# Optimization experiments

Hardware: AMD Instinct MI355X
Metric: run time of the kernel (lower is better)

## Reference

```python
import jax, jax.numpy as jnp
import numpy as np

K = 8  # search_range in sample_wise_recolor
BIG = 1e30


def setup_inputs() -> dict:
    key = jax.random.key(0)
    ks = jax.random.split(key, 6)
    L, N = 16384, 10000  # L: upsampled candidate voxels (multiple of 8), N: target points
    pred_F = jax.random.normal(ks[0], (L,), jnp.float32)
    cand_xyz = jax.random.normal(ks[1], (L, 3), jnp.float32) * 50.0
    cand_rgb = jax.random.uniform(ks[2], (L, 3), jnp.float32)
    tgt_xyz = jax.random.normal(ks[3], (N, 3), jnp.float32) * 50.0
    tgt_rgb = jax.random.uniform(ks[4], (N, 3), jnp.float32)
    keep_target = jax.random.randint(ks[5], (L,), 0, 2, jnp.int32)
    return {"pred_F": pred_F, "cand_xyz": cand_xyz, "cand_rgb": cand_rgb,
            "tgt_xyz": tgt_xyz, "tgt_rgb": tgt_rgb, "keep_target": keep_target,
            "points_num": 8192}


def _get_keep(pred, points_num):
    # local-max mask over groups of 8 children (scatter of per-row argmax)
    L = pred.shape[0]
    p8 = pred.reshape(-1, 8)
    rows = jnp.arange(p8.shape[0])
    is_local_max = jnp.zeros(p8.shape, dtype=bool).at[rows, jnp.argmax(p8, axis=1)].set(True).reshape(-1)
    # kthvalue over the non-local-max subset: local-max entries pushed to +inf so the
    # k-th smallest of the full sorted array equals the k-th smallest of the subset.
    k = L - points_num  # static python int
    vals = jnp.where(is_local_max, jnp.inf, pred)
    threshold = jnp.sort(vals)[k - 1]
    return (pred > threshold) | is_local_max


def _pairwise_sqdist(a, b):
    # a: [P,3], b: [Q,3] -> [P,Q] squared distances
    a2 = jnp.sum(a * a, axis=1)
    b2 = jnp.sum(b * b, axis=1)
    d2 = a2[:, None] + b2[None, :] - 2.0 * (a @ b.T)
    return jnp.maximum(d2, 0.0)


def _recolor_loss(cand_xyz, rgb, keep, tgt_xyz, tgt_rgb):
    L = cand_xyz.shape[0]
    N = tgt_xyz.shape[0]
    d2 = _pairwise_sqdist(tgt_xyz, cand_xyz)  # [N, L]

    # ---- recolor_backward: KNN from each target point into kept candidates ----
    d_masked = jnp.where(keep[None, :], d2, BIG)
    neg_d, idx = jax.lax.top_k(-d_masked, K)  # [N, K]
    d = -neg_d
    zero_mask = d == 0.0
    min_mask = (d == jnp.min(d, axis=1, keepdims=True)) & ~jnp.any(zero_mask, axis=1)[:, None]
    w = jnp.where(min_mask, 1.0 / jnp.sqrt(jnp.maximum(d, 1e-30)), 0.0)  # [N, K]

    flat_idx = idx.reshape(-1)
    num = jnp.zeros((L, 3), rgb.dtype).at[flat_idx].add((tgt_rgb[:, None, :] * w[:, :, None]).reshape(-1, 3))
    den = jnp.zeros((L,), rgb.dtype).at[flat_idx].add(w.reshape(-1))
    has_den = den != 0.0
    recolored = jnp.where(has_den[:, None], num / jnp.where(has_den, den, 1.0)[:, None], 0.0)

    # exact-match (zero-distance) targets overwrite; scatter with safe out-of-range dummy row
    safe_idx = jnp.where(zero_mask, idx, L).reshape(-1)
    tgt_exp = jnp.broadcast_to(tgt_rgb[:, None, :], (N, K, 3)).reshape(-1, 3)
    recolored = jnp.concatenate([recolored, jnp.zeros((1, 3), rgb.dtype)], 0).at[safe_idx].set(tgt_exp)[:L]
    empty = jnp.concatenate([~has_den, jnp.zeros((1,), bool)], 0).at[safe_idx].set(False)[:L]
    empty = empty & keep  # only kept candidates matter

    # ---- recolor_forward: kept candidates with no color yet pull from nearest targets ----
    neg_df, idxf = jax.lax.top_k(-d2.T, K)  # [L, K]
    df = -neg_df
    mf = df == jnp.min(df, axis=1, keepdims=True)
    rec_fwd = jnp.sum(tgt_rgb[idxf] * mf[:, :, None], axis=1) / jnp.sum(mf, axis=1, keepdims=True).astype(rgb.dtype)
    recolored = jnp.where(empty[:, None], rec_fwd, recolored)

    # L1 loss over kept candidates only; recolor target is no-grad in the original
    recolored = jax.lax.stop_gradient(recolored)
    return jnp.sum(jnp.where(keep[:, None], jnp.abs(rgb - recolored), 0.0))


def reference(pred_F, cand_xyz, cand_rgb, tgt_xyz, tgt_rgb, keep_target, points_num):
    keep = _get_keep(jax.lax.stop_gradient(pred_F), points_num)  # @torch.no_grad
    # coord recon loss: BCE-with-logits, reduction='sum'
    t = keep_target.astype(pred_F.dtype)
    coord_loss = jnp.sum(jnp.maximum(pred_F, 0.0) - pred_F * t + jnp.log1p(jnp.exp(-jnp.abs(pred_F))))
    # inverse_transform_for_color in training mode: x * 255
    rgb = cand_rgb * 255.0
    rgb_loss = _recolor_loss(cand_xyz, rgb, keep, tgt_xyz, tgt_rgb)
    return jnp.stack([coord_loss, rgb_loss])
```

## Files before the change

### kernel.cpp

```cpp
#include <hip/hip_runtime.h>
#include <hip/hip_bf16.h>


#define SCAN_T 256
typedef unsigned long long ull;

__global__ __launch_bounds__(256) void k_prep(
    const float* __restrict__ pred, const float* __restrict__ txyz,
    float4* __restrict__ ttile, float4* __restrict__ numden,
    int* __restrict__ zerohit, ull* __restrict__ tmin, ull* __restrict__ fmin,
    unsigned int* __restrict__ key, unsigned char* __restrict__ islm,
    int* __restrict__ counters, float* __restrict__ out, int L, int N) {
  int gidx = blockIdx.x * 256 + threadIdx.x;
  int gsz = (int)gridDim.x * 256;
  for (int i = gidx; i < N; i += gsz) {
    float x = txyz[3*i], y = txyz[3*i+1], z = txyz[3*i+2];
    ttile[i] = make_float4(x, y, z, fmaf(x, x, fmaf(y, y, z * z)));
    tmin[i] = ~0ull;
  }
  for (int i = gidx; i < L; i += gsz) {
    numden[i] = make_float4(0.f, 0.f, 0.f, 0.f);
    zerohit[i] = 0;
    fmin[i] = ~0ull;
  }
  if (gidx < 8) counters[gidx] = 0;
  if (gidx < 2) out[gidx] = 0.f;
  int ngroups = L >> 3;
  for (int g = gidx; g < ngroups; g += gsz) {
    const float4* pv = (const float4*)pred + (size_t)g * 2;
    float4 a = pv[0], b = pv[1];
    float v[8] = {a.x, a.y, a.z, a.w, b.x, b.y, b.z, b.w};
    int bi = 0; float bv = v[0];
    #pragma unroll
    for (int j = 1; j < 8; ++j) if (v[j] > bv) { bv = v[j]; bi = j; }
    unsigned int kk[8];
    ull lmpack = 0ull;
    #pragma unroll
    for (int j = 0; j < 8; ++j) {
      unsigned int fb = __float_as_uint(v[j]);
      unsigned int mk = (fb & 0x80000000u) ? ~fb : (fb | 0x80000000u);
      if (j == bi) { mk = 0xFF800000u; lmpack |= 1ull << (8 * j); }
      kk[j] = mk;
    }
    ((uint4*)key)[g*2]   = make_uint4(kk[0], kk[1], kk[2], kk[3]);
    ((uint4*)key)[g*2+1] = make_uint4(kk[4], kk[5], kk[6], kk[7]);
    *(ull*)(islm + (size_t)g * 8) = lmpack;
  }
}

__device__ __forceinline__ void select_bin(
    unsigned int* hist, int nb, unsigned int rank,
    unsigned int* sB, unsigned int* sR, int tid) {
  if (tid < 64) {
    int g = nb >> 6;
    unsigned int sum = 0;
    for (int j = 0; j < g; ++j) sum += hist[tid * g + j];
    unsigned int incl = sum;
    for (int o = 1; o < 64; o <<= 1) {
      unsigned int v = __shfl_up(incl, o);
      if (tid >= o) incl += v;
    }
    unsigned int excl = incl - sum;
    bool cond = (rank >= excl) && (rank < incl);
    unsigned long long bal = __ballot(cond);
    int first = __ffsll((long long)bal) - 1;
    if (tid == first) {
      unsigned int r = rank - excl, cum = 0;
      for (int j = 0; j < g; ++j) {
        unsigned int c = hist[tid * g + j];
        if (r < cum + c) { *sB = (unsigned int)(tid * g + j); *sR = r - cum; break; }
        cum += c;
      }
    }
  }
}

__global__ __launch_bounds__(256) void k_sel(
    const unsigned int* __restrict__ key, const int* __restrict__ pnum_p,
    float* __restrict__ thr_out, int L) {
  __shared__ unsigned int hist[2048];
  __shared__ unsigned int sB, sR;
  int tid = threadIdx.x;
  unsigned int rank = (unsigned int)(L - pnum_p[0] - 1);
  const uint4* k4 = (const uint4*)key;
  int n4 = L >> 2;
  for (int b = tid; b < 2048; b += 256) hist[b] = 0u;
  __syncthreads();
  for (int i = tid; i < n4; i += 256) {
    uint4 v = k4[i];
    atomicAdd(&hist[v.x >> 21], 1u); atomicAdd(&hist[v.y >> 21], 1u);
    atomicAdd(&hist[v.z >> 21], 1u); atomicAdd(&hist[v.w >> 21], 1u);
  }
  __syncthreads();
  select_bin(hist, 2048, rank, &sB, &sR, tid);
  __syncthreads();
  unsigned int B1 = sB, R1 = sR;
  for (int b = tid; b < 2048; b += 256) hist[b] = 0u;
  __syncthreads();
  for (int i = tid; i < n4; i += 256) {
    uint4 v = k4[i];
    if ((v.x >> 21) == B1) atomicAdd(&hist[(v.x >> 10) & 2047u], 1u);
    if ((v.y >> 21) == B1) atomicAdd(&hist[(v.y >> 10) & 2047u], 1u);
    if ((v.z >> 21) == B1) atomicAdd(&hist[(v.z >> 10) & 2047u], 1u);
    if ((v.w >> 21) == B1) atomicAdd(&hist[(v.w >> 10) & 2047u], 1u);
  }
  __syncthreads();
  select_bin(hist, 2048, R1, &sB, &sR, tid);
  __syncthreads();
  unsigned int B2 = sB, R2 = sR;
  for (int b = tid; b < 1024; b += 256) hist[b] = 0u;
  __syncthreads();
  unsigned int top22 = (B1 << 11) | B2;
  for (int i = tid; i < n4; i += 256) {
    uint4 v = k4[i];
    if ((v.x >> 10) == top22) atomicAdd(&hist[v.x & 1023u], 1u);
    if ((v.y >> 10) == top22) atomicAdd(&hist[v.y & 1023u], 1u);
    if ((v.z >> 10) == top22) atomicAdd(&hist[v.z & 1023u], 1u);
    if ((v.w >> 10) == top22) atomicAdd(&hist[v.w & 1023u], 1u);
  }
  __syncthreads();
  select_bin(hist, 1024, R2, &sB, &sR, tid);
  __syncthreads();
  if (tid == 0) {
    unsigned int fkey = (B1 << 21) | (B2 << 10) | sB;
    unsigned int fb = (fkey & 0x80000000u) ? (fkey & 0x7FFFFFFFu) : ~fkey;
    thr_out[0] = __uint_as_float(fb);
  }
}

__global__ __launch_bounds__(256) void k_keepc(
    const float* __restrict__ pred, const unsigned char* __restrict__ islm,
    const float* __restrict__ thr_p, const float* __restrict__ cxyz,
    const int* __restrict__ ktgt, int* __restrict__ keep,
    float4* __restrict__ klist, int* __restrict__ kidx,
    int* __restrict__ counters, float* __restrict__ out, int L) {
  int i = blockIdx.x * 256 + threadIdx.x;
  float thr = thr_p[0];
  float term = 0.f;
  if (i < L) {
    float p = pred[i];
    bool kp = (p > thr) || islm[i];
    keep[i] = kp ? 1 : 0;
    if (kp) {
      int pos = atomicAdd(&counters[0], 1);
      float x = cxyz[3*i], y = cxyz[3*i+1], z = cxyz[3*i+2];
      klist[pos] = make_float4(x, y, z, fmaf(x, x, fmaf(y, y, z * z)));
      kidx[pos] = i;
    }
    float t = (float)ktgt[i];
    term = fmaxf(p, 0.f) - p * t + log1pf(expf(-fabsf(p)));
  }
  for (int o = 32; o > 0; o >>= 1) term += __shfl_down(term, o);
  if ((threadIdx.x & 63) == 0) atomicAdd(&out[0], term);
}

__global__ __launch_bounds__(SCAN_T) void k_scan2(
    const float* __restrict__ txyz, const float4* __restrict__ klist,
    const int* __restrict__ kidx, const float4* __restrict__ ttile,
    const int* __restrict__ counters, ull* __restrict__ tmin,
    ull* __restrict__ fmin, int L, int N, int YB) {
  __shared__ float4 tile[SCAN_T];
  int tid = threadIdx.x, x = blockIdx.x, y = blockIdx.y;
  int kc = counters[0];

  if (y < YB) {
    int c0 = y * 512;
    if (x * 256 >= N || c0 >= kc) return;
    int c1 = min(c0 + 512, kc);
    int t = x * 256 + tid;
    bool act = t < N;
    float tx = 0.f, ty = 0.f, tz = 0.f;
    if (act) { tx = txyz[3*t]; ty = txyz[3*t+1]; tz = txyz[3*t+2]; }
    float ntx = -2.f * tx, nty = -2.f * ty, ntz = -2.f * tz;
    float best = 3e38f; int bpos = -1;
    for (int tb = c0; tb < c1; tb += SCAN_T) {
      int cnt = min(SCAN_T, c1 - tb);
      if (tid < cnt) tile[tid] = klist[tb + tid];
      __syncthreads();
      #pragma unroll 8
      for (int c = 0; c < cnt; ++c) {
        float4 cd = tile[c];
        float d = fmaf(ntx, cd.x, cd.w);
        d = fmaf(nty, cd.y, d);
        d = fmaf(ntz, cd.z, d);
        if (d < best) { best = d; bpos = tb + c; }
      }
      __syncthreads();
    }
    if (act && bpos >= 0) {
      float4 cd = klist[bpos];
      float dx = tx - cd.x, dy = ty - cd.y, dz = tz - cd.z;
      float dtrue = fmaf(dx, dx, fmaf(dy, dy, dz * dz));
      ull pack = ((ull)__float_as_uint(dtrue) << 32) | (unsigned int)kidx[bpos];
      atomicMin(&tmin[t], pack);
    }
  } else {
    int t0 = (y - YB) * 512;
    if (x * 256 >= kc) return;
    int t1 = min(t0 + 512, N);
    int e = x * 256 + tid;
    bool act = e < kc;
    float cx = 0.f, cy = 0.f, cz = 0.f, c2 = 0.f;
    int l = 0;
    if (act) {
      float4 cd = klist[e];
      cx = cd.x; cy = cd.y; cz = cd.z; c2 = cd.w;
      l = kidx[e];
    }
    float ncx = -2.f * cx, ncy = -2.f * cy, ncz = -2.f * cz;
    float best = 3e38f; int bidx = 0;
    for (int tb = t0; tb < t1; tb += SCAN_T) {
      int cnt = min(SCAN_T, t1 - tb);
      if (tid < cnt) tile[tid] = ttile[tb + tid];
      __syncthreads();
      #pragma unroll 8
      for (int c = 0; c < cnt; ++c) {
        float4 td = tile[c];
        float d = fmaf(ncx, td.x, td.w);
        d = fmaf(ncy, td.y, d);
        d = fmaf(ncz, td.z, d);
        if (d < best) { best = d; bidx = tb + c; }
      }
      __syncthreads();
    }
    if (act) {
      float dkey = fmaxf(best + c2, 0.f);
      ull pack = ((ull)__float_as_uint(dkey) << 32) | (unsigned int)bidx;
      atomicMin(&fmin[l], pack);
    }
  }
}

__global__ __launch_bounds__(256) void k_scatter(
    const float* __restrict__ trgb, const ull* __restrict__ tmin,
    float4* __restrict__ numden, int* __restrict__ zerohit,
    float4* __restrict__ zcolor, int N) {
  int t = blockIdx.x * 256 + threadIdx.x;
  if (t >= N) return;
  ull pack = tmin[t];
  float d = __uint_as_float((unsigned int)(pack >> 32));
  int idx = (int)(pack & 0xFFFFFFFFull);
  float r = trgb[3*t], g = trgb[3*t+1], b = trgb[3*t+2];
  if (d == 0.0f) {
    zerohit[idx] = 1;
    zcolor[idx] = make_float4(r, g, b, 0.f);
  } else {
    float w = 1.0f / sqrtf(fmaxf(d, 1e-30f));
    atomicAdd(&numden[idx].x, r * w);
    atomicAdd(&numden[idx].y, g * w);
    atomicAdd(&numden[idx].z, b * w);
    atomicAdd(&numden[idx].w, w);
  }
}

__global__ __launch_bounds__(256) void k_loss(
    const float* __restrict__ crgb, const float* __restrict__ trgb,
    const int* __restrict__ keep, const float4* __restrict__ numden,
    const int* __restrict__ zerohit, const float4* __restrict__ zcolor,
    const ull* __restrict__ fmin, float* __restrict__ out, int L) {
  int l = blockIdx.x * 256 + threadIdx.x;
  float loss = 0.f;
  if (l < L && keep[l]) {
    float rr, rg, rb;
    if (zerohit[l]) {
      float4 z = zcolor[l]; rr = z.x; rg = z.y; rb = z.z;
    } else {
      float4 nd = numden[l];
      if (nd.w != 0.f) { rr = nd.x / nd.w; rg = nd.y / nd.w; rb = nd.z / nd.w; }
      else {
        int ti = (int)(fmin[l] & 0xFFFFFFFFull);
        rr = trgb[3*ti]; rg = trgb[3*ti+1]; rb = trgb[3*ti+2];
      }
    }
    float sr = crgb[3*l]*255.f, sg = crgb[3*l+1]*255.f, sb = crgb[3*l+2]*255.f;
    loss = fabsf(sr - rr) + fabsf(sg - rg) + fabsf(sb - rb);
  }
  for (int o = 32; o > 0; o >>= 1) loss += __shfl_down(loss, o);
  if ((threadIdx.x & 63) == 0) atomicAdd(&out[1], loss);
}

extern "C" void kernel_launch(void* const* d_in, const int* in_sizes, int n_in,
                              void* d_out, int out_size, void* d_ws, size_t ws_size,
                              hipStream_t stream) {
  const float* pred = (const float*)d_in[0];
  const float* cxyz = (const float*)d_in[1];
  const float* crgb = (const float*)d_in[2];
  const float* txyz = (const float*)d_in[3];
  const float* trgb = (const float*)d_in[4];
  const int*   ktgt = (const int*)d_in[5];
  const int*   pnum = (const int*)d_in[6];
  int L = in_sizes[0];
  int N = in_sizes[3] / 3;

  char* ws = (char*)d_ws;
  size_t off = 0;
  float4* klist  = (float4*)(ws + off);   off += (size_t)L * 16;
  float4* ttile  = (float4*)(ws + off);   off += (size_t)((N + 3) & ~3) * 16;
  float4* numden = (float4*)(ws + off);   off += (size_t)L * 16;
  float4* zcolor = (float4*)(ws + off);   off += (size_t)L * 16;
  unsigned int* key = (unsigned int*)(ws + off); off += (size_t)L * 4;
  ull* tmin      = (ull*)(ws + off);      off += (size_t)((N + 1) & ~1) * 8;
  ull* fmin      = (ull*)(ws + off);      off += (size_t)L * 8;
  int* keep      = (int*)(ws + off);      off += (size_t)L * 4;
  int* kidx      = (int*)(ws + off);      off += (size_t)L * 4;
  int* zerohit   = (int*)(ws + off);      off += (size_t)L * 4;
  float* thr_slot = (float*)(ws + off);   off += 16;
  int* counters  = (int*)(ws + off);      off += 256;
  unsigned char* islm = (unsigned char*)(ws + off); off += ((size_t)L + 15) & ~15ull;
  float* out = (float*)d_out;

  int nbL = (L + 255) / 256;
  int nbN = (N + 255) / 256;
  int YB = (L + 511) / 512;
  int YF = (N + 511) / 512;
  int mx = max(L, N);

  k_prep<<<(mx + 255) / 256, 256, 0, stream>>>(
      pred, txyz, ttile, numden, zerohit, tmin, fmin, key, islm, counters, out, L, N);

  k_sel<<<1, 256, 0, stream>>>(key, pnum, thr_slot, L);

  k_keepc<<<nbL, 256, 0, stream>>>(
      pred, islm, thr_slot, cxyz, ktgt, keep, klist, kidx, counters, out, L);

  dim3 gs(nbL, YB + YF);
  k_scan2<<<gs, SCAN_T, 0, stream>>>(
      txyz, klist, kidx, ttile, counters, tmin, fmin, L, N, YB);

  k_scatter<<<nbN, 256, 0, stream>>>(trgb, tmin, numden, zerohit, zcolor, N);

  k_loss<<<nbL, 256, 0, stream>>>(
      crgb, trgb, keep, numden, zerohit, zcolor, fmin, out, L);
}
```

Before: 140.3 us.

## Replace split-grid NN scan with wave-per-query scan and shuffle reductions

The nearest-neighbour search changes from one thread per query over 512-candidate chunks with 64-bit atomicMin merges to one wavefront handling four queries. Lanes stride over the full candidate list in 1024-entry shared tiles, then combine results with xor-shuffle argmin reductions, so the atomics, the init of tmin/fmin and the packed 64-bit keys go away. The forward direction now stores a plain int index per candidate. The grid becomes a 1D launch of roughly N/16 + L/16 blocks, each scanning the whole list. This trades atomic traffic and chunk-level parallelism for more blocks, each doing longer serial work.

New measurement: 144.1 us. +2.7%, slower.

```diff
diff --git a/kernel.cpp b/kernel.cpp
--- a/kernel.cpp
+++ b/kernel.cpp
@@ -2,26 +2,24 @@
 #include <hip/hip_bf16.h>
 
 
-#define SCAN_T 256
+#define CH 1024
 typedef unsigned long long ull;
 
 __global__ __launch_bounds__(256) void k_prep(
     const float* __restrict__ pred, const float* __restrict__ txyz,
     float4* __restrict__ ttile, float4* __restrict__ numden,
-    int* __restrict__ zerohit, ull* __restrict__ tmin, ull* __restrict__ fmin,
-    unsigned int* __restrict__ key, unsigned char* __restrict__ islm,
-    int* __restrict__ counters, float* __restrict__ out, int L, int N) {
+    int* __restrict__ zerohit, unsigned int* __restrict__ key,
+    unsigned char* __restrict__ islm, int* __restrict__ counters,
+    float* __restrict__ out, int L, int N) {
   int gidx = blockIdx.x * 256 + threadIdx.x;
   int gsz = (int)gridDim.x * 256;
   for (int i = gidx; i < N; i += gsz) {
     float x = txyz[3*i], y = txyz[3*i+1], z = txyz[3*i+2];
     ttile[i] = make_float4(x, y, z, fmaf(x, x, fmaf(y, y, z * z)));
-    tmin[i] = ~0ull;
   }
   for (int i = gidx; i < L; i += gsz) {
     numden[i] = make_float4(0.f, 0.f, 0.f, 0.f);
     zerohit[i] = 0;
-    fmin[i] = ~0ull;
   }
   if (gidx < 8) counters[gidx] = 0;
   if (gidx < 2) out[gidx] = 0.f;
@@ -154,79 +152,101 @@
   if ((threadIdx.x & 63) == 0) atomicAdd(&out[0], term);
 }
 
-__global__ __launch_bounds__(SCAN_T) void k_scan2(
+__global__ __launch_bounds__(256) void k_scanw(
     const float* __restrict__ txyz, const float4* __restrict__ klist,
     const int* __restrict__ kidx, const float4* __restrict__ ttile,
     const int* __restrict__ counters, ull* __restrict__ tmin,
-    ull* __restrict__ fmin, int L, int N, int YB) {
-  __shared__ float4 tile[SCAN_T];
-  int tid = threadIdx.x, x = blockIdx.x, y = blockIdx.y;
+    int* __restrict__ fidx, int L, int N, int NBW) {
+  __shared__ float4 sb[CH];
+  int tid = threadIdx.x;
+  int lane = tid & 63;
+  int wv = tid >> 6;
   int kc = counters[0];
-
-  if (y < YB) {
-    int c0 = y * 512;
-    if (x * 256 >= N || c0 >= kc) return;
-    int c1 = min(c0 + 512, kc);
-    int t = x * 256 + tid;
-    bool act = t < N;
-    float tx = 0.f, ty = 0.f, tz = 0.f;
-    if (act) { tx = txyz[3*t]; ty = txyz[3*t+1]; tz = txyz[3*t+2]; }
-    float ntx = -2.f * tx, nty = -2.f * ty, ntz = -2.f * tz;
-    float best = 3e38f; int bpos = -1;
-    for (int tb = c0; tb < c1; tb += SCAN_T) {
-      int cnt = min(SCAN_T, c1 - tb);
-      if (tid < cnt) tile[tid] = klist[tb + tid];
-      __syncthreads();
-      #pragma unroll 8
-      for (int c = 0; c < cnt; ++c) {
-        float4 cd = tile[c];
-        float d = fmaf(ntx, cd.x, cd.w);
-        d = fmaf(nty, cd.y, d);
-        d = fmaf(ntz, cd.z, d);
-        if (d < best) { best = d; bpos = tb + c; }
+  int bid = blockIdx.x;
+
+  float q0x, q0y, q0z, q1x, q1y, q1z, q2x, q2y, q2z, q3x, q3y, q3z;
+  const float4* list; int listn; int q0;
+  if (bid < NBW) {
+    q0 = bid * 16 + wv * 4;
+    int a = min(q0, N - 1), b = min(q0 + 1, N - 1),
+        c = min(q0 + 2, N - 1), d = min(q0 + 3, N - 1);
+    q0x = txyz[3*a]; q0y = txyz[3*a+1]; q0z = txyz[3*a+2];
+    q1x = txyz[3*b]; q1y = txyz[3*b+1]; q1z = txyz[3*b+2];
+    q2x = txyz[3*c]; q2y = txyz[3*c+1]; q2z = txyz[3*c+2];
+    q3x = txyz[3*d]; q3y = txyz[3*d+1]; q3z = txyz[3*d+2];
+    list = klist; listn = kc;
+  } else {
+    int eb = (bid - NBW) * 16;
+    if (eb >= kc) return;
+    q0 = eb + wv * 4;
+    int a = min(q0, kc - 1), b = min(q0 + 1, kc - 1),
+        c = min(q0 + 2, kc - 1), d = min(q0 + 3, kc - 1);
+    float4 A = klist[a], B = klist[b], C = klist[c], D = klist[d];
+    q0x = A.x; q0y = A.y; q0z = A.z;
+    q1x = B.x; q1y = B.y; q1z = B.z;
+    q2x = C.x; q2y = C.y; q2z = C.z;
+    q3x = D.x; q3y = D.y; q3z = D.z;
+    list = ttile; listn = N;
+  }
+  float n0x = -2.f*q0x, n0y = -2.f*q0y, n0z = -2.f*q0z;
+  float n1x = -2.f*q1x, n1y = -2.f*q1y, n1z = -2.f*q1z;
+  float n2x = -2.f*q2x, n2y = -2.f*q2y, n2z = -2.f*q2z;
+  float n3x = -2.f*q3x, n3y = -2.f*q3y, n3z = -2.f*q3z;
+  float b0 = 3e38f, b1 = 3e38f, b2 = 3e38f, b3 = 3e38f;
+  int i0 = 0, i1 = 0, i2 = 0, i3 = 0;
+
+  for (int tile = 0; tile < listn; tile += CH) {
+    int cnt = min(CH, listn - tile);
+    int cntp = (cnt + 63) & ~63;
+    for (int j = tid; j < cntp; j += 256)
+      sb[j] = (j < cnt) ? list[tile + j] : make_float4(0.f, 0.f, 0.f, 3e38f);
+    __syncthreads();
+    #pragma unroll 2
+    for (int i = lane; i < cntp; i += 64) {
+      float4 A = sb[i];
+      int c = tile + i;
+      float d0 = fmaf(n0x, A.x, A.w); d0 = fmaf(n0y, A.y, d0); d0 = fmaf(n0z, A.z, d0);
+      float d1 = fmaf(n1x, A.x, A.w); d1 = fmaf(n1y, A.y, d1); d1 = fmaf(n1z, A.z, d1);
+      float d2 = fmaf(n2x, A.x, A.w); d2 = fmaf(n2y, A.y, d2); d2 = fmaf(n2z, A.z, d2);
+      float d3 = fmaf(n3x, A.x, A.w); d3 = fmaf(n3y, A.y, d3); d3 = fmaf(n3z, A.z, d3);
+      if (d0 < b0) { b0 = d0; i0 = c; }
+      if (d1 < b1) { b1 = d1; i1 = c; }
+      if (d2 < b2) { b2 = d2; i2 = c; }
+      if (d3 < b3) { b3 = d3; i3 = c; }
+    }
+    __syncthreads();
+  }
+  #pragma unroll
+  for (int o = 32; o > 0; o >>= 1) {
+    float ob; int oi;
+    ob = __shfl_xor(b0, o); oi = __shfl_xor(i0, o);
+    if (ob < b0 || (ob == b0 && oi < i0)) { b0 = ob; i0 = oi; }
+    ob = __shfl_xor(b1, o); oi = __shfl_xor(i1, o);
+    if (ob < b1 || (ob == b1 && oi < i1)) { b1 = ob; i1 = oi; }
+    ob = __shfl_xor(b2, o); oi = __shfl_xor(i2, o);
+    if (ob < b2 || (ob == b2 && oi < i2)) { b2 = ob; i2 = oi; }
+    ob = __shfl_xor(b3, o); oi = __shfl_xor(i3, o);
+    if (ob < b3 || (ob == b3 && oi < i3)) { b3 = ob; i3 = oi; }
+  }
+  if (lane == 0) {
+    int ii[4] = {i0, i1, i2, i3};
+    if (bid < NBW) {
+      #pragma unroll
+      for (int j = 0; j < 4; ++j) {
+        int t = q0 + j;
+        if (t < N) {
+          float4 cd = klist[ii[j]];
+          float dx = txyz[3*t] - cd.x, dy = txyz[3*t+1] - cd.y, dz = txyz[3*t+2] - cd.z;
+          float dtrue = fmaf(dx, dx, fmaf(dy, dy, dz * dz));
+          tmin[t] = ((ull)__float_as_uint(dtrue) << 32) | (unsigned int)kidx[ii[j]];
+        }
       }
-      __syncthreads();
-    }
-    if (act && bpos >= 0) {
-      float4 cd = klist[bpos];
-      float dx = tx - cd.x, dy = ty - cd.y, dz = tz - cd.z;
-      float dtrue = fmaf(dx, dx, fmaf(dy, dy, dz * dz));
-      ull pack = ((ull)__float_as_uint(dtrue) << 32) | (unsigned int)kidx[bpos];
-      atomicMin(&tmin[t], pack);
-    }
-  } else {
-    int t0 = (y - YB) * 512;
-    if (x * 256 >= kc) return;
-    int t1 = min(t0 + 512, N);
-    int e = x * 256 + tid;
-    bool act = e < kc;
-    float cx = 0.f, cy = 0.f, cz = 0.f, c2 = 0.f;
-    int l = 0;
-    if (act) {
-      float4 cd = klist[e];
-      cx = cd.x; cy = cd.y; cz = cd.z; c2 = cd.w;
-      l = kidx[e];
-    }
-    float ncx = -2.f * cx, ncy = -2.f * cy, ncz = -2.f * cz;
-    float best = 3e38f; int bidx = 0;
-    for (int tb = t0; tb < t1; tb += SCAN_T) {
-      int cnt = min(SCAN_T, t1 - tb);
-      if (tid < cnt) tile[tid] = ttile[tb + tid];
-      __syncthreads();
-      #pragma unroll 8
-      for (int c = 0; c < cnt; ++c) {
-        float4 td = tile[c];
-        float d = fmaf(ncx, td.x, td.w);
-        d = fmaf(ncy, td.y, d);
-        d = fmaf(ncz, td.z, d);
-        if (d < best) { best = d; bidx = tb + c; }
+    } else {
+      #pragma unroll
+      for (int j = 0; j < 4; ++j) {
+        int e = q0 + j;
+        if (e < kc) fidx[kidx[e]] = ii[j];
       }
-      __syncthreads();
-    }
-    if (act) {
-      float dkey = fmaxf(best + c2, 0.f);
-      ull pack = ((ull)__float_as_uint(dkey) << 32) | (unsigned int)bidx;
-      atomicMin(&fmin[l], pack);
     }
   }
 }
@@ -257,7 +277,7 @@
     const float* __restrict__ crgb, const float* __restrict__ trgb,
     const int* __restrict__ keep, const float4* __restrict__ numden,
     const int* __restrict__ zerohit, const float4* __restrict__ zcolor,
-    const ull* __restrict__ fmin, float* __restrict__ out, int L) {
+    const int* __restrict__ fidx, float* __restrict__ out, int L) {
   int l = blockIdx.x * 256 + threadIdx.x;
   float loss = 0.f;
   if (l < L && keep[l]) {
@@ -268,7 +288,7 @@
       float4 nd = numden[l];
       if (nd.w != 0.f) { rr = nd.x / nd.w; rg = nd.y / nd.w; rb = nd.z / nd.w; }
       else {
-        int ti = (int)(fmin[l] & 0xFFFFFFFFull);
+        int ti = fidx[l];
         rr = trgb[3*ti]; rg = trgb[3*ti+1]; rb = trgb[3*ti+2];
       }
     }
@@ -300,10 +320,10 @@
   float4* zcolor = (float4*)(ws + off);   off += (size_t)L * 16;
   unsigned int* key = (unsigned int*)(ws + off); off += (size_t)L * 4;
   ull* tmin      = (ull*)(ws + off);      off += (size_t)((N + 1) & ~1) * 8;
-  ull* fmin      = (ull*)(ws + off);      off += (size_t)L * 8;
   int* keep      = (int*)(ws + off);      off += (size_t)L * 4;
   int* kidx      = (int*)(ws + off);      off += (size_t)L * 4;
   int* zerohit   = (int*)(ws + off);      off += (size_t)L * 4;
+  int* fidx      = (int*)(ws + off);      off += (size_t)L * 4;
   float* thr_slot = (float*)(ws + off);   off += 16;
   int* counters  = (int*)(ws + off);      off += 256;
   unsigned char* islm = (unsigned char*)(ws + off); off += ((size_t)L + 15) & ~15ull;
@@ -311,24 +331,23 @@
 
   int nbL = (L + 255) / 256;
   int nbN = (N + 255) / 256;
-  int YB = (L + 511) / 512;
-  int YF = (N + 511) / 512;
+  int NBW = (N + 15) / 16;
+  int NFW = (L + 15) / 16;
   int mx = max(L, N);
 
   k_prep<<<(mx + 255) / 256, 256, 0, stream>>>(
-      pred, txyz, ttile, numden, zerohit, tmin, fmin, key, islm, counters, out, L, N);
+      pred, txyz, ttile, numden, zerohit, key, islm, counters, out, L, N);
 
   k_sel<<<1, 256, 0, stream>>>(key, pnum, thr_slot, L);
 
   k_keepc<<<nbL, 256, 0, stream>>>(
       pred, islm, thr_slot, cxyz, ktgt, keep, klist, kidx, counters, out, L);
 
-  dim3 gs(nbL, YB + YF);
-  k_scan2<<<gs, SCAN_T, 0, stream>>>(
-      txyz, klist, kidx, ttile, counters, tmin, fmin, L, N, YB);
+  k_scanw<<<NBW + NFW, 256, 0, stream>>>(
+      txyz, klist, kidx, ttile, counters, tmin, fidx, L, N, NBW);
 
   k_scatter<<<nbN, 256, 0, stream>>>(trgb, tmin, numden, zerohit, zcolor, N);
 
   k_loss<<<nbL, 256, 0, stream>>>(
-      crgb, trgb, keep, numden, zerohit, zcolor, fmin, out, L);
-}
+      crgb, trgb, keep, numden, zerohit, zcolor, fidx, out, L);
+}
```
